# Kernel tuning notes

Measured on AMD Instinct MI355X. Metric: run time of the kernel, lower is better.

Reference implementation:

```python
import jax, jax.numpy as jnp
import numpy as np

B, NF, NT = 8, 4096, 4096
D_IN, D_HID, D_OUT, D_V = 3, 128, 32, 16


def mlp(x, W1, b1, W2, b2):
    # x: [B, N, D_IN] -> [B, N, D_OUT]
    h = jax.nn.relu(jnp.einsum('bni,ih->bnh', x, W1) + b1)
    return jnp.einsum('bnh,ho->bno', h, W2) + b2


def l1_cdist(a, b):
    # a: [B, N, d], b: [B, M, d] -> [B, N, M], sum_d |a-b|
    # scan over the small feature dim d to avoid a [B,N,M,d] intermediate
    aT = jnp.moveaxis(a, -1, 0)  # [d, B, N]
    bT = jnp.moveaxis(b, -1, 0)  # [d, B, M]

    def step(acc, ab):
        ai, bi = ab
        return acc + jnp.abs(ai[:, :, None] - bi[:, None, :]), None

    init = jnp.zeros((a.shape[0], a.shape[1], b.shape[1]), dtype=a.dtype)
    acc, _ = jax.lax.scan(step, init, (aT, bT))
    return acc


def setup_inputs() -> dict:
    key = jax.random.key(0)
    ks = jax.random.split(key, 11)
    s1 = 1.0 / np.sqrt(D_IN)
    s2 = 1.0 / np.sqrt(D_HID)
    return {
        'coords_f': jax.random.normal(ks[0], (B, NF, D_IN), jnp.float32),
        'values_f': jax.random.normal(ks[1], (B, NF, D_V), jnp.float32),
        'coords_t': jax.random.normal(ks[2], (B, NT, D_IN), jnp.float32),
        'Wk1': jax.random.uniform(ks[3], (D_IN, D_HID), jnp.float32, -s1, s1),
        'bk1': jax.random.uniform(ks[4], (D_HID,), jnp.float32, -s1, s1),
        'Wk2': jax.random.uniform(ks[5], (D_HID, D_OUT), jnp.float32, -s2, s2),
        'bk2': jax.random.uniform(ks[6], (D_OUT,), jnp.float32, -s2, s2),
        'Wq1': jax.random.uniform(ks[7], (D_IN, D_HID), jnp.float32, -s1, s1),
        'bq1': jax.random.uniform(ks[8], (D_HID,), jnp.float32, -s1, s1),
        'Wq2': jax.random.uniform(ks[9], (D_HID, D_OUT), jnp.float32, -s2, s2),
        'bq2': jax.random.uniform(ks[10], (D_OUT,), jnp.float32, -s2, s2),
    }


def reference(coords_f, values_f, coords_t, Wk1, bk1, Wk2, bk2, Wq1, bq1, Wq2, bq2):
    Wk = mlp(coords_f, Wk1, bk1, Wk2, bk2)  # [B, NF, D_OUT]
    Wq = mlp(coords_t, Wq1, bq1, Wq2, bq2)  # [B, NT, D_OUT]
    score = l1_cdist(Wk, Wq)                # [B, NF, NT]
    attn = jax.nn.softmax(-(score ** 2) / 2.0, axis=1)  # softmax over NF
    # 'bij,bik->bjk': [B,NF,NT] x [B,NF,V] -> [B,NT,V]
    return jnp.einsum('bij,bik->bjk', attn, values_f)
```

## Files before the change

### kernel.cpp

```cpp
#include <hip/hip_runtime.h>

#define B 8
#define NF 4096
#define NT 4096
#define D_HID 128
#define D_OUT 32
#define D_V 16
#define TILE_I 64

__device__ inline float fast_exp2(float x) {
#if __has_builtin(__builtin_amdgcn_exp2f)
  return __builtin_amdgcn_exp2f(x);
#else
  return exp2f(x);
#endif
}

__global__ __launch_bounds__(64) void mlp_kernel(
    const float* __restrict__ x, const float* __restrict__ W1,
    const float* __restrict__ b1, const float* __restrict__ W2,
    const float* __restrict__ b2, float* __restrict__ out) {
  __shared__ float sW1[3 * D_HID];
  __shared__ float sb1[D_HID];
  __shared__ float sW2[D_HID * D_OUT];
  __shared__ float sb2[D_OUT];
  const int tid = threadIdx.x;
  for (int idx = tid; idx < D_HID * D_OUT; idx += 64) sW2[idx] = W2[idx];
  for (int idx = tid; idx < 3 * D_HID; idx += 64) sW1[idx] = W1[idx];
  for (int idx = tid; idx < D_HID; idx += 64) sb1[idx] = b1[idx];
  if (tid < D_OUT) sb2[tid] = b2[tid];
  __syncthreads();

  const int t = blockIdx.x * 64 + tid;
  const float x0 = x[t * 3 + 0];
  const float x1 = x[t * 3 + 1];
  const float x2 = x[t * 3 + 2];
  float acc[D_OUT];
#pragma unroll
  for (int o = 0; o < D_OUT; ++o) acc[o] = sb2[o];
#pragma unroll 4
  for (int h = 0; h < D_HID; ++h) {
    float hv = fmaf(x2, sW1[2 * D_HID + h],
               fmaf(x1, sW1[1 * D_HID + h],
               fmaf(x0, sW1[0 * D_HID + h], sb1[h])));
    hv = fmaxf(hv, 0.0f);
    const float4* w2r = reinterpret_cast<const float4*>(&sW2[h * D_OUT]);
#pragma unroll
    for (int o4 = 0; o4 < D_OUT / 4; ++o4) {
      const float4 w = w2r[o4];
      acc[o4 * 4 + 0] = fmaf(hv, w.x, acc[o4 * 4 + 0]);
      acc[o4 * 4 + 1] = fmaf(hv, w.y, acc[o4 * 4 + 1]);
      acc[o4 * 4 + 2] = fmaf(hv, w.z, acc[o4 * 4 + 2]);
      acc[o4 * 4 + 3] = fmaf(hv, w.w, acc[o4 * 4 + 3]);
    }
  }
  float* op = out + (size_t)t * D_OUT;
#pragma unroll
  for (int o = 0; o < D_OUT; o += 4) {
    float4 w = make_float4(acc[o], acc[o + 1], acc[o + 2], acc[o + 3]);
    *reinterpret_cast<float4*>(op + o) = w;
  }
}

__global__ __launch_bounds__(256, 3) void attn_kernel(
    const float* __restrict__ Wk, const float* __restrict__ Wq,
    const float* __restrict__ Vf, float* __restrict__ partial,
    int nchunks, int chlen) {
  __shared__ float4 sTile[2][768];
  const int tid = threadIdx.x;
  const int j0 = blockIdx.x * 512 + tid;
  const int j1 = j0 + 256;
  const int b = blockIdx.y;
  const int c = blockIdx.z;
  const int i0 = c * chlen;
  const int ntiles = chlen / TILE_I;

  float q[2][D_OUT];
  {
    const float* qp0 = Wq + ((size_t)b * NT + j0) * D_OUT;
    const float* qp1 = Wq + ((size_t)b * NT + j1) * D_OUT;
#pragma unroll
    for (int d = 0; d < D_OUT; d += 4) {
      float4 t4 = *reinterpret_cast<const float4*>(qp0 + d);
      q[0][d + 0] = t4.x; q[0][d + 1] = t4.y; q[0][d + 2] = t4.z; q[0][d + 3] = t4.w;
      float4 u4 = *reinterpret_cast<const float4*>(qp1 + d);
      q[1][d + 0] = u4.x; q[1][d + 1] = u4.y; q[1][d + 2] = u4.z; q[1][d + 3] = u4.w;
    }
  }

  constexpr float C2 = -0.72134752044448170368f;

  float m0 = -1e30f, m1 = -1e30f;
  float l0 = 0.0f, l1 = 0.0f;
  float acc[2][D_V];
#pragma unroll
  for (int s = 0; s < 2; ++s)
#pragma unroll
    for (int k = 0; k < D_V; ++k) acc[s][k] = 0.0f;

  const float4* gK4 = reinterpret_cast<const float4*>(Wk + ((size_t)b * NF + i0) * D_OUT);
  const float4* gV4 = reinterpret_cast<const float4*>(Vf + ((size_t)b * NF + i0) * D_V);

  {
    float4 f0 = gK4[tid];
    float4 f1 = gK4[256 + tid];
    float4 f2 = gV4[tid];
    sTile[0][tid] = f0;
    sTile[0][256 + tid] = f1;
    sTile[0][512 + tid] = f2;
  }
  __syncthreads();

  for (int t = 0; t < ntiles; ++t) {
    const int cur = t & 1;
    float4 f0, f1, f2;
    const bool more = (t + 1 < ntiles);
    if (more) {
      f0 = gK4[(size_t)(t + 1) * 512 + tid];
      f1 = gK4[(size_t)(t + 1) * 512 + 256 + tid];
      f2 = gV4[(size_t)(t + 1) * 256 + tid];
    }
    const float4* kb4 = &sTile[cur][0];
    const float4* vb4 = &sTile[cur][512];
    for (int r = 0; r < TILE_I; ++r) {
      const float4 k0 = kb4[0];
      const float4 k1 = kb4[1];
      const float4 k2 = kb4[2];
      const float4 k3 = kb4[3];
      float a0 = fabsf(k0.x - q[0][0]);
      float b0 = fabsf(k0.x - q[1][0]);
      float a1 = fabsf(k0.y - q[0][1]);
      float b1 = fabsf(k0.y - q[1][1]);
      float a2 = fabsf(k0.z - q[0][2]);
      float b2 = fabsf(k0.z - q[1][2]);
      float a3 = fabsf(k0.w - q[0][3]);
      float b3 = fabsf(k0.w - q[1][3]);
      a0 += fabsf(k1.x - q[0][4]);  b0 += fabsf(k1.x - q[1][4]);
      a1 += fabsf(k1.y - q[0][5]);  b1 += fabsf(k1.y - q[1][5]);
      a2 += fabsf(k1.z - q[0][6]);  b2 += fabsf(k1.z - q[1][6]);
      a3 += fabsf(k1.w - q[0][7]);  b3 += fabsf(k1.w - q[1][7]);
      a0 += fabsf(k2.x - q[0][8]);  b0 += fabsf(k2.x - q[1][8]);
      a1 += fabsf(k2.y - q[0][9]);  b1 += fabsf(k2.y - q[1][9]);
      a2 += fabsf(k2.z - q[0][10]); b2 += fabsf(k2.z - q[1][10]);
      a3 += fabsf(k2.w - q[0][11]); b3 += fabsf(k2.w - q[1][11]);
      a0 += fabsf(k3.x - q[0][12]); b0 += fabsf(k3.x - q[1][12]);
      a1 += fabsf(k3.y - q[0][13]); b1 += fabsf(k3.y - q[1][13]);
      a2 += fabsf(k3.z - q[0][14]); b2 += fabsf(k3.z - q[1][14]);
      a3 += fabsf(k3.w - q[0][15]); b3 += fabsf(k3.w - q[1][15]);
      const float4 k4 = kb4[4];
      const float4 k5 = kb4[5];
      const float4 k6 = kb4[6];
      const float4 k7 = kb4[7];
      kb4 += 8;
      a0 += fabsf(k4.x - q[0][16]); b0 += fabsf(k4.x - q[1][16]);
      a1 += fabsf(k4.y - q[0][17]); b1 += fabsf(k4.y - q[1][17]);
      a2 += fabsf(k4.z - q[0][18]); b2 += fabsf(k4.z - q[1][18]);
      a3 += fabsf(k4.w - q[0][19]); b3 += fabsf(k4.w - q[1][19]);
      a0 += fabsf(k5.x - q[0][20]); b0 += fabsf(k5.x - q[1][20]);
      a1 += fabsf(k5.y - q[0][21]); b1 += fabsf(k5.y - q[1][21]);
      a2 += fabsf(k5.z - q[0][22]); b2 += fabsf(k5.z - q[1][22]);
      a3 += fabsf(k5.w - q[0][23]); b3 += fabsf(k5.w - q[1][23]);
      a0 += fabsf(k6.x - q[0][24]); b0 += fabsf(k6.x - q[1][24]);
      a1 += fabsf(k6.y - q[0][25]); b1 += fabsf(k6.y - q[1][25]);
      a2 += fabsf(k6.z - q[0][26]); b2 += fabsf(k6.z - q[1][26]);
      a3 += fabsf(k6.w - q[0][27]); b3 += fabsf(k6.w - q[1][27]);
      a0 += fabsf(k7.x - q[0][28]); b0 += fabsf(k7.x - q[1][28]);
      a1 += fabsf(k7.y - q[0][29]); b1 += fabsf(k7.y - q[1][29]);
      a2 += fabsf(k7.z - q[0][30]); b2 += fabsf(k7.z - q[1][30]);
      a3 += fabsf(k7.w - q[0][31]); b3 += fabsf(k7.w - q[1][31]);
      const float dist0 = (a0 + a1) + (a2 + a3);
      const float dist1 = (b0 + b1) + (b2 + b3);

      const float d20 = dist0 * dist0;
      const float d21 = dist1 * dist1;
      float parg0 = fmaf(C2, d20, -m0);
      float parg1 = fmaf(C2, d21, -m1);
      if (__any(fmaxf(parg0, parg1) > 4.0f)) {
        const float s20 = C2 * d20;
        const float mn0 = fmaxf(m0, s20);
        const float al0 = fast_exp2(m0 - mn0);
        l0 *= al0;
#pragma unroll
        for (int k = 0; k < D_V; ++k) acc[0][k] *= al0;
        m0 = mn0;
        parg0 = s20 - mn0;
        const float s21 = C2 * d21;
        const float mn1 = fmaxf(m1, s21);
        const float al1 = fast_exp2(m1 - mn1);
        l1 *= al1;
#pragma unroll
        for (int k = 0; k < D_V; ++k) acc[1][k] *= al1;
        m1 = mn1;
        parg1 = s21 - mn1;
      }
      const float p0 = fast_exp2(parg0);
      const float p1 = fast_exp2(parg1);
      l0 += p0;
      l1 += p1;

      {
        const float4 v0 = vb4[0];
        const float4 v1 = vb4[1];
        acc[0][0]  = fmaf(p0, v0.x, acc[0][0]);   acc[1][0]  = fmaf(p1, v0.x, acc[1][0]);
        acc[0][1]  = fmaf(p0, v0.y, acc[0][1]);   acc[1][1]  = fmaf(p1, v0.y, acc[1][1]);
        acc[0][2]  = fmaf(p0, v0.z, acc[0][2]);   acc[1][2]  = fmaf(p1, v0.z, acc[1][2]);
        acc[0][3]  = fmaf(p0, v0.w, acc[0][3]);   acc[1][3]  = fmaf(p1, v0.w, acc[1][3]);
        acc[0][4]  = fmaf(p0, v1.x, acc[0][4]);   acc[1][4]  = fmaf(p1, v1.x, acc[1][4]);
        acc[0][5]  = fmaf(p0, v1.y, acc[0][5]);   acc[1][5]  = fmaf(p1, v1.y, acc[1][5]);
        acc[0][6]  = fmaf(p0, v1.z, acc[0][6]);   acc[1][6]  = fmaf(p1, v1.z, acc[1][6]);
        acc[0][7]  = fmaf(p0, v1.w, acc[0][7]);   acc[1][7]  = fmaf(p1, v1.w, acc[1][7]);
      }
      {
        const float4 v2 = vb4[2];
        const float4 v3 = vb4[3];
        vb4 += 4;
        acc[0][8]  = fmaf(p0, v2.x, acc[0][8]);   acc[1][8]  = fmaf(p1, v2.x, acc[1][8]);
        acc[0][9]  = fmaf(p0, v2.y, acc[0][9]);   acc[1][9]  = fmaf(p1, v2.y, acc[1][9]);
        acc[0][10] = fmaf(p0, v2.z, acc[0][10]);  acc[1][10] = fmaf(p1, v2.z, acc[1][10]);
        acc[0][11] = fmaf(p0, v2.w, acc[0][11]);  acc[1][11] = fmaf(p1, v2.w, acc[1][11]);
        acc[0][12] = fmaf(p0, v3.x, acc[0][12]);  acc[1][12] = fmaf(p1, v3.x, acc[1][12]);
        acc[0][13] = fmaf(p0, v3.y, acc[0][13]);  acc[1][13] = fmaf(p1, v3.y, acc[1][13]);
        acc[0][14] = fmaf(p0, v3.z, acc[0][14]);  acc[1][14] = fmaf(p1, v3.z, acc[1][14]);
        acc[0][15] = fmaf(p0, v3.w, acc[0][15]);  acc[1][15] = fmaf(p1, v3.w, acc[1][15]);
      }
    }
    if (more) {
      const int nxt = cur ^ 1;
      sTile[nxt][tid] = f0;
      sTile[nxt][256 + tid] = f1;
      sTile[nxt][512 + tid] = f2;
    }
    __syncthreads();
  }

  const size_t fstride = (size_t)nchunks * B * NT;
  float* ps0 = partial + ((size_t)c * B + b) * NT + j0;
  float* ps1 = partial + ((size_t)c * B + b) * NT + j1;
  ps0[0] = m0;
  ps1[0] = m1;
  ps0[fstride] = l0;
  ps1[fstride] = l1;
#pragma unroll
  for (int k = 0; k < D_V; ++k) {
    ps0[(size_t)(2 + k) * fstride] = acc[0][k];
    ps1[(size_t)(2 + k) * fstride] = acc[1][k];
  }
}

__global__ __launch_bounds__(256) void combine_kernel(
    const float* __restrict__ partial, float* __restrict__ out, int nchunks) {
  const int t = blockIdx.x * 256 + threadIdx.x;
  const size_t fstride = (size_t)nchunks * B * NT;
  float M = -1e30f;
  for (int c = 0; c < nchunks; ++c)
    M = fmaxf(M, partial[(size_t)c * (B * NT) + t]);
  float L = 0.0f;
  float acc[D_V];
#pragma unroll
  for (int k = 0; k < D_V; ++k) acc[k] = 0.0f;
  for (int c = 0; c < nchunks; ++c) {
    const size_t base = (size_t)c * (B * NT) + t;
    const float w = fast_exp2(partial[base] - M);
    L = fmaf(w, partial[fstride + base], L);
#pragma unroll
    for (int k = 0; k < D_V; ++k)
      acc[k] = fmaf(w, partial[(size_t)(2 + k) * fstride + base], acc[k]);
  }
  const float inv = 1.0f / L;
  float* op = out + (size_t)t * D_V;
#pragma unroll
  for (int k = 0; k < D_V; ++k) op[k] = acc[k] * inv;
}

extern "C" void kernel_launch(void* const* d_in, const int* in_sizes, int n_in,
                              void* d_out, int out_size, void* d_ws, size_t ws_size,
                              hipStream_t stream) {
  const float* coords_f = (const float*)d_in[0];
  const float* values_f = (const float*)d_in[1];
  const float* coords_t = (const float*)d_in[2];
  const float* Wk1 = (const float*)d_in[3];
  const float* bk1 = (const float*)d_in[4];
  const float* Wk2 = (const float*)d_in[5];
  const float* bk2 = (const float*)d_in[6];
  const float* Wq1 = (const float*)d_in[7];
  const float* bq1 = (const float*)d_in[8];
  const float* Wq2 = (const float*)d_in[9];
  const float* bq2 = (const float*)d_in[10];
  float* out = (float*)d_out;

  float* Wk = (float*)d_ws;
  float* Wq = Wk + (size_t)B * NF * D_OUT;
  float* partial = Wq + (size_t)B * NT * D_OUT;

  const size_t fixed = (size_t)(B * NF * D_OUT + B * NT * D_OUT) * sizeof(float);
  int nchunks = 32;
  while (nchunks > 1 &&
         fixed + (size_t)B * NT * nchunks * 18 * sizeof(float) > ws_size)
    nchunks >>= 1;
  const int chlen = NF / nchunks;

  hipLaunchKernelGGL(mlp_kernel, dim3(B * NF / 64), dim3(64), 0, stream,
                     coords_f, Wk1, bk1, Wk2, bk2, Wk);
  hipLaunchKernelGGL(mlp_kernel, dim3(B * NT / 64), dim3(64), 0, stream,
                     coords_t, Wq1, bq1, Wq2, bq2, Wq);
  hipLaunchKernelGGL(attn_kernel, dim3(NT / 512, B, nchunks), dim3(256), 0, stream,
                     Wk, Wq, values_f, partial, nchunks, chlen);
  hipLaunchKernelGGL(combine_kernel, dim3(B * NT / 256), dim3(256), 0, stream,
                     partial, out, nchunks);
}
```

Measured before the change: 429.1 us.

## Split NF into 128-row chunks loaded once, dropping tile double-buffering

Each block now handles a fixed 128-row chunk of keys and values, loaded into shared memory once before the loop. This replaces the double-buffered 64-row tile pipeline and its per-tile barriers. The chunk count grows to 32 regardless of workspace size, which gives more blocks and parallelism but enlarges the partial buffer and the combine work. Occupancy hints are raised to 4 blocks per CU, and the combine kernel uses 128-thread blocks. The fixed chunk count also drops the workspace-size check, so a small workspace could overflow.

```diff
diff --git a/kernel.cpp b/kernel.cpp
--- a/kernel.cpp
+++ b/kernel.cpp
@@ -6,7 +6,7 @@
 #define D_HID 128
 #define D_OUT 32
 #define D_V 16
-#define TILE_I 64
+#define CHLEN 128
 
 __device__ inline float fast_exp2(float x) {
 #if __has_builtin(__builtin_amdgcn_exp2f)
@@ -62,29 +62,38 @@
   }
 }
 
-__global__ __launch_bounds__(256, 3) void attn_kernel(
+__global__ __launch_bounds__(256, 4) void attn_kernel(
     const float* __restrict__ Wk, const float* __restrict__ Wq,
     const float* __restrict__ Vf, float* __restrict__ partial,
-    int nchunks, int chlen) {
-  __shared__ float4 sTile[2][768];
+    int nchunks) {
+  __shared__ float4 sK[CHLEN * 8];
+  __shared__ float4 sV[CHLEN * 4];
   const int tid = threadIdx.x;
-  const int j0 = blockIdx.x * 512 + tid;
-  const int j1 = j0 + 256;
   const int b = blockIdx.y;
   const int c = blockIdx.z;
-  const int i0 = c * chlen;
-  const int ntiles = chlen / TILE_I;
+  const int i0 = c * CHLEN;
+  const int j0 = blockIdx.x * 512 + tid;
+
+  {
+    const float4* gK4 =
+        reinterpret_cast<const float4*>(Wk + ((size_t)b * NF + i0) * D_OUT);
+    const float4* gV4 =
+        reinterpret_cast<const float4*>(Vf + ((size_t)b * NF + i0) * D_V);
+#pragma unroll
+    for (int i = 0; i < 4; ++i) sK[tid + 256 * i] = gK4[tid + 256 * i];
+#pragma unroll
+    for (int i = 0; i < 2; ++i) sV[tid + 256 * i] = gV4[tid + 256 * i];
+  }
 
   float q[2][D_OUT];
-  {
-    const float* qp0 = Wq + ((size_t)b * NT + j0) * D_OUT;
-    const float* qp1 = Wq + ((size_t)b * NT + j1) * D_OUT;
+#pragma unroll
+  for (int s = 0; s < 2; ++s) {
+    const float* qp = Wq + ((size_t)b * NT + j0 + s * 256) * D_OUT;
 #pragma unroll
     for (int d = 0; d < D_OUT; d += 4) {
-      float4 t4 = *reinterpret_cast<const float4*>(qp0 + d);
-      q[0][d + 0] = t4.x; q[0][d + 1] = t4.y; q[0][d + 2] = t4.z; q[0][d + 3] = t4.w;
-      float4 u4 = *reinterpret_cast<const float4*>(qp1 + d);
-      q[1][d + 0] = u4.x; q[1][d + 1] = u4.y; q[1][d + 2] = u4.z; q[1][d + 3] = u4.w;
+      float4 t4 = *reinterpret_cast<const float4*>(qp + d);
+      q[s][d + 0] = t4.x; q[s][d + 1] = t4.y;
+      q[s][d + 2] = t4.z; q[s][d + 3] = t4.w;
     }
   }
 
@@ -98,158 +107,129 @@
 #pragma unroll
     for (int k = 0; k < D_V; ++k) acc[s][k] = 0.0f;
 
-  const float4* gK4 = reinterpret_cast<const float4*>(Wk + ((size_t)b * NF + i0) * D_OUT);
-  const float4* gV4 = reinterpret_cast<const float4*>(Vf + ((size_t)b * NF + i0) * D_V);
-
+  __syncthreads();
+
+  for (int r = 0; r < CHLEN; ++r) {
+    const float4* kp = &sK[r * 8];
+    const float4 k0 = kp[0];
+    const float4 k1 = kp[1];
+    const float4 k2 = kp[2];
+    const float4 k3 = kp[3];
+    float a0 = fabsf(k0.x - q[0][0]);
+    float b0 = fabsf(k0.x - q[1][0]);
+    float a1 = fabsf(k0.y - q[0][1]);
+    float b1 = fabsf(k0.y - q[1][1]);
+    float a2 = fabsf(k0.z - q[0][2]);
+    float b2 = fabsf(k0.z - q[1][2]);
+    float a3 = fabsf(k0.w - q[0][3]);
+    float b3 = fabsf(k0.w - q[1][3]);
+    a0 += fabsf(k1.x - q[0][4]);  b0 += fabsf(k1.x - q[1][4]);
+    a1 += fabsf(k1.y - q[0][5]);  b1 += fabsf(k1.y - q[1][5]);
+    a2 += fabsf(k1.z - q[0][6]);  b2 += fabsf(k1.z - q[1][6]);
+    a3 += fabsf(k1.w - q[0][7]);  b3 += fabsf(k1.w - q[1][7]);
+    a0 += fabsf(k2.x - q[0][8]);  b0 += fabsf(k2.x - q[1][8]);
+    a1 += fabsf(k2.y - q[0][9]);  b1 += fabsf(k2.y - q[1][9]);
+    a2 += fabsf(k2.z - q[0][10]); b2 += fabsf(k2.z - q[1][10]);
+    a3 += fabsf(k2.w - q[0][11]); b3 += fabsf(k2.w - q[1][11]);
+    a0 += fabsf(k3.x - q[0][12]); b0 += fabsf(k3.x - q[1][12]);
+    a1 += fabsf(k3.y - q[0][13]); b1 += fabsf(k3.y - q[1][13]);
+    a2 += fabsf(k3.z - q[0][14]); b2 += fabsf(k3.z - q[1][14]);
+    a3 += fabsf(k3.w - q[0][15]); b3 += fabsf(k3.w - q[1][15]);
+    const float4 k4 = kp[4];
+    const float4 k5 = kp[5];
+    const float4 k6 = kp[6];
+    const float4 k7 = kp[7];
+    a0 += fabsf(k4.x - q[0][16]); b0 += fabsf(k4.x - q[1][16]);
+    a1 += fabsf(k4.y - q[0][17]); b1 += fabsf(k4.y - q[1][17]);
+    a2 += fabsf(k4.z - q[0][18]); b2 += fabsf(k4.z - q[1][18]);
+    a3 += fabsf(k4.w - q[0][19]); b3 += fabsf(k4.w - q[1][19]);
+    a0 += fabsf(k5.x - q[0][20]); b0 += fabsf(k5.x - q[1][20]);
+    a1 += fabsf(k5.y - q[0][21]); b1 += fabsf(k5.y - q[1][21]);
+    a2 += fabsf(k5.z - q[0][22]); b2 += fabsf(k5.z - q[1][22]);
+    a3 += fabsf(k5.w - q[0][23]); b3 += fabsf(k5.w - q[1][23]);
+    a0 += fabsf(k6.x - q[0][24]); b0 += fabsf(k6.x - q[1][24]);
+    a1 += fabsf(k6.y - q[0][25]); b1 += fabsf(k6.y - q[1][25]);
+    a2 += fabsf(k6.z - q[0][26]); b2 += fabsf(k6.z - q[1][26]);
+    a3 += fabsf(k6.w - q[0][27]); b3 += fabsf(k6.w - q[1][27]);
+    a0 += fabsf(k7.x - q[0][28]); b0 += fabsf(k7.x - q[1][28]);
+    a1 += fabsf(k7.y - q[0][29]); b1 += fabsf(k7.y - q[1][29]);
+    a2 += fabsf(k7.z - q[0][30]); b2 += fabsf(k7.z - q[1][30]);
+    a3 += fabsf(k7.w - q[0][31]); b3 += fabsf(k7.w - q[1][31]);
+    const float dist0 = (a0 + a1) + (a2 + a3);
+    const float dist1 = (b0 + b1) + (b2 + b3);
+
+    const float d20 = dist0 * dist0;
+    const float d21 = dist1 * dist1;
+    float parg0 = fmaf(C2, d20, -m0);
+    float parg1 = fmaf(C2, d21, -m1);
+    if (__any(fmaxf(parg0, parg1) > 4.0f)) {
+      const float s20 = C2 * d20;
+      const float mn0 = fmaxf(m0, s20);
+      const float al0 = fast_exp2(m0 - mn0);
+      l0 *= al0;
+#pragma unroll
+      for (int k = 0; k < D_V; ++k) acc[0][k] *= al0;
+      m0 = mn0;
+      parg0 = s20 - mn0;
+      const float s21 = C2 * d21;
+      const float mn1 = fmaxf(m1, s21);
+      const float al1 = fast_exp2(m1 - mn1);
+      l1 *= al1;
+#pragma unroll
+      for (int k = 0; k < D_V; ++k) acc[1][k] *= al1;
+      m1 = mn1;
+      parg1 = s21 - mn1;
+    }
+    const float p0 = fast_exp2(parg0);
+    const float p1 = fast_exp2(parg1);
+    l0 += p0;
+    l1 += p1;
+
+    {
+      const float4 v0 = sV[r * 4 + 0];
+      const float4 v1 = sV[r * 4 + 1];
+      acc[0][0] = fmaf(p0, v0.x, acc[0][0]);  acc[1][0] = fmaf(p1, v0.x, acc[1][0]);
+      acc[0][1] = fmaf(p0, v0.y, acc[0][1]);  acc[1][1] = fmaf(p1, v0.y, acc[1][1]);
+      acc[0][2] = fmaf(p0, v0.z, acc[0][2]);  acc[1][2] = fmaf(p1, v0.z, acc[1][2]);
+      acc[0][3] = fmaf(p0, v0.w, acc[0][3]);  acc[1][3] = fmaf(p1, v0.w, acc[1][3]);
+      acc[0][4] = fmaf(p0, v1.x, acc[0][4]);  acc[1][4] = fmaf(p1, v1.x, acc[1][4]);
+      acc[0][5] = fmaf(p0, v1.y, acc[0][5]);  acc[1][5] = fmaf(p1, v1.y, acc[1][5]);
+      acc[0][6] = fmaf(p0, v1.z, acc[0][6]);  acc[1][6] = fmaf(p1, v1.z, acc[1][6]);
+      acc[0][7] = fmaf(p0, v1.w, acc[0][7]);  acc[1][7] = fmaf(p1, v1.w, acc[1][7]);
+    }
+    {
+      const float4 v2 = sV[r * 4 + 2];
+      const float4 v3 = sV[r * 4 + 3];
+      acc[0][8]  = fmaf(p0, v2.x, acc[0][8]);   acc[1][8]  = fmaf(p1, v2.x, acc[1][8]);
+      acc[0][9]  = fmaf(p0, v2.y, acc[0][9]);   acc[1][9]  = fmaf(p1, v2.y, acc[1][9]);
+      acc[0][10] = fmaf(p0, v2.z, acc[0][10]);  acc[1][10] = fmaf(p1, v2.z, acc[1][10]);
+      acc[0][11] = fmaf(p0, v2.w, acc[0][11]);  acc[1][11] = fmaf(p1, v2.w, acc[1][11]);
+      acc[0][12] = fmaf(p0, v3.x, acc[0][12]);  acc[1][12] = fmaf(p1, v3.x, acc[1][12]);
+      acc[0][13] = fmaf(p0, v3.y, acc[0][13]);  acc[1][13] = fmaf(p1, v3.y, acc[1][13]);
+      acc[0][14] = fmaf(p0, v3.z, acc[0][14]);  acc[1][14] = fmaf(p1, v3.z, acc[1][14]);
+      acc[0][15] = fmaf(p0, v3.w, acc[0][15]);  acc[1][15] = fmaf(p1, v3.w, acc[1][15]);
+    }
+  }
+
+  const size_t fstride = (size_t)nchunks * B * NT;
+  const size_t base = ((size_t)c * B + b) * NT;
   {
-    float4 f0 = gK4[tid];
-    float4 f1 = gK4[256 + tid];
-    float4 f2 = gV4[tid];
-    sTile[0][tid] = f0;
-    sTile[0][256 + tid] = f1;
-    sTile[0][512 + tid] = f2;
-  }
-  __syncthreads();
-
-  for (int t = 0; t < ntiles; ++t) {
-    const int cur = t & 1;
-    float4 f0, f1, f2;
-    const bool more = (t + 1 < ntiles);
-    if (more) {
-      f0 = gK4[(size_t)(t + 1) * 512 + tid];
-      f1 = gK4[(size_t)(t + 1) * 512 + 256 + tid];
-      f2 = gV4[(size_t)(t + 1) * 256 + tid];
-    }
-    const float4* kb4 = &sTile[cur][0];
-    const float4* vb4 = &sTile[cur][512];
-    for (int r = 0; r < TILE_I; ++r) {
-      const float4 k0 = kb4[0];
-      const float4 k1 = kb4[1];
-      const float4 k2 = kb4[2];
-      const float4 k3 = kb4[3];
-      float a0 = fabsf(k0.x - q[0][0]);
-      float b0 = fabsf(k0.x - q[1][0]);
-      float a1 = fabsf(k0.y - q[0][1]);
-      float b1 = fabsf(k0.y - q[1][1]);
-      float a2 = fabsf(k0.z - q[0][2]);
-      float b2 = fabsf(k0.z - q[1][2]);
-      float a3 = fabsf(k0.w - q[0][3]);
-      float b3 = fabsf(k0.w - q[1][3]);
-      a0 += fabsf(k1.x - q[0][4]);  b0 += fabsf(k1.x - q[1][4]);
-      a1 += fabsf(k1.y - q[0][5]);  b1 += fabsf(k1.y - q[1][5]);
-      a2 += fabsf(k1.z - q[0][6]);  b2 += fabsf(k1.z - q[1][6]);
-      a3 += fabsf(k1.w - q[0][7]);  b3 += fabsf(k1.w - q[1][7]);
-      a0 += fabsf(k2.x - q[0][8]);  b0 += fabsf(k2.x - q[1][8]);
-      a1 += fabsf(k2.y - q[0][9]);  b1 += fabsf(k2.y - q[1][9]);
-      a2 += fabsf(k2.z - q[0][10]); b2 += fabsf(k2.z - q[1][10]);
-      a3 += fabsf(k2.w - q[0][11]); b3 += fabsf(k2.w - q[1][11]);
-      a0 += fabsf(k3.x - q[0][12]); b0 += fabsf(k3.x - q[1][12]);
-      a1 += fabsf(k3.y - q[0][13]); b1 += fabsf(k3.y - q[1][13]);
-      a2 += fabsf(k3.z - q[0][14]); b2 += fabsf(k3.z - q[1][14]);
-      a3 += fabsf(k3.w - q[0][15]); b3 += fabsf(k3.w - q[1][15]);
-      const float4 k4 = kb4[4];
-      const float4 k5 = kb4[5];
-      const float4 k6 = kb4[6];
-      const float4 k7 = kb4[7];
-      kb4 += 8;
-      a0 += fabsf(k4.x - q[0][16]); b0 += fabsf(k4.x - q[1][16]);
-      a1 += fabsf(k4.y - q[0][17]); b1 += fabsf(k4.y - q[1][17]);
-      a2 += fabsf(k4.z - q[0][18]); b2 += fabsf(k4.z - q[1][18]);
-      a3 += fabsf(k4.w - q[0][19]); b3 += fabsf(k4.w - q[1][19]);
-      a0 += fabsf(k5.x - q[0][20]); b0 += fabsf(k5.x - q[1][20]);
-      a1 += fabsf(k5.y - q[0][21]); b1 += fabsf(k5.y - q[1][21]);
-      a2 += fabsf(k5.z - q[0][22]); b2 += fabsf(k5.z - q[1][22]);
-      a3 += fabsf(k5.w - q[0][23]); b3 += fabsf(k5.w - q[1][23]);
-      a0 += fabsf(k6.x - q[0][24]); b0 += fabsf(k6.x - q[1][24]);
-      a1 += fabsf(k6.y - q[0][25]); b1 += fabsf(k6.y - q[1][25]);
-      a2 += fabsf(k6.z - q[0][26]); b2 += fabsf(k6.z - q[1][26]);
-      a3 += fabsf(k6.w - q[0][27]); b3 += fabsf(k6.w - q[1][27]);
-      a0 += fabsf(k7.x - q[0][28]); b0 += fabsf(k7.x - q[1][28]);
-      a1 += fabsf(k7.y - q[0][29]); b1 += fabsf(k7.y - q[1][29]);
-      a2 += fabsf(k7.z - q[0][30]); b2 += fabsf(k7.z - q[1][30]);
-      a3 += fabsf(k7.w - q[0][31]); b3 += fabsf(k7.w - q[1][31]);
-      const float dist0 = (a0 + a1) + (a2 + a3);
-      const float dist1 = (b0 + b1) + (b2 + b3);
-
-      const float d20 = dist0 * dist0;
-      const float d21 = dist1 * dist1;
-      float parg0 = fmaf(C2, d20, -m0);
-      float parg1 = fmaf(C2, d21, -m1);
-      if (__any(fmaxf(parg0, parg1) > 4.0f)) {
-        const float s20 = C2 * d20;
-        const float mn0 = fmaxf(m0, s20);
-        const float al0 = fast_exp2(m0 - mn0);
-        l0 *= al0;
-#pragma unroll
-        for (int k = 0; k < D_V; ++k) acc[0][k] *= al0;
-        m0 = mn0;
-        parg0 = s20 - mn0;
-        const float s21 = C2 * d21;
-        const float mn1 = fmaxf(m1, s21);
-        const float al1 = fast_exp2(m1 - mn1);
-        l1 *= al1;
-#pragma unroll
-        for (int k = 0; k < D_V; ++k) acc[1][k] *= al1;
-        m1 = mn1;
-        parg1 = s21 - mn1;
-      }
-      const float p0 = fast_exp2(parg0);
-      const float p1 = fast_exp2(parg1);
-      l0 += p0;
-      l1 += p1;
-
-      {
-        const float4 v0 = vb4[0];
-        const float4 v1 = vb4[1];
-        acc[0][0]  = fmaf(p0, v0.x, acc[0][0]);   acc[1][0]  = fmaf(p1, v0.x, acc[1][0]);
-        acc[0][1]  = fmaf(p0, v0.y, acc[0][1]);   acc[1][1]  = fmaf(p1, v0.y, acc[1][1]);
-        acc[0][2]  = fmaf(p0, v0.z, acc[0][2]);   acc[1][2]  = fmaf(p1, v0.z, acc[1][2]);
-        acc[0][3]  = fmaf(p0, v0.w, acc[0][3]);   acc[1][3]  = fmaf(p1, v0.w, acc[1][3]);
-        acc[0][4]  = fmaf(p0, v1.x, acc[0][4]);   acc[1][4]  = fmaf(p1, v1.x, acc[1][4]);
-        acc[0][5]  = fmaf(p0, v1.y, acc[0][5]);   acc[1][5]  = fmaf(p1, v1.y, acc[1][5]);
-        acc[0][6]  = fmaf(p0, v1.z, acc[0][6]);   acc[1][6]  = fmaf(p1, v1.z, acc[1][6]);
-        acc[0][7]  = fmaf(p0, v1.w, acc[0][7]);   acc[1][7]  = fmaf(p1, v1.w, acc[1][7]);
-      }
-      {
-        const float4 v2 = vb4[2];
-        const float4 v3 = vb4[3];
-        vb4 += 4;
-        acc[0][8]  = fmaf(p0, v2.x, acc[0][8]);   acc[1][8]  = fmaf(p1, v2.x, acc[1][8]);
-        acc[0][9]  = fmaf(p0, v2.y, acc[0][9]);   acc[1][9]  = fmaf(p1, v2.y, acc[1][9]);
-        acc[0][10] = fmaf(p0, v2.z, acc[0][10]);  acc[1][10] = fmaf(p1, v2.z, acc[1][10]);
-        acc[0][11] = fmaf(p0, v2.w, acc[0][11]);  acc[1][11] = fmaf(p1, v2.w, acc[1][11]);
-        acc[0][12] = fmaf(p0, v3.x, acc[0][12]);  acc[1][12] = fmaf(p1, v3.x, acc[1][12]);
-        acc[0][13] = fmaf(p0, v3.y, acc[0][13]);  acc[1][13] = fmaf(p1, v3.y, acc[1][13]);
-        acc[0][14] = fmaf(p0, v3.z, acc[0][14]);  acc[1][14] = fmaf(p1, v3.z, acc[1][14]);
-        acc[0][15] = fmaf(p0, v3.w, acc[0][15]);  acc[1][15] = fmaf(p1, v3.w, acc[1][15]);
-      }
-    }
-    if (more) {
-      const int nxt = cur ^ 1;
-      sTile[nxt][tid] = f0;
-      sTile[nxt][256 + tid] = f1;
-      sTile[nxt][512 + tid] = f2;
-    }
-    __syncthreads();
-  }
-
-  const size_t fstride = (size_t)nchunks * B * NT;
-  float* ps0 = partial + ((size_t)c * B + b) * NT + j0;
-  float* ps1 = partial + ((size_t)c * B + b) * NT + j1;
-  ps0[0] = m0;
-  ps1[0] = m1;
-  ps0[fstride] = l0;
-  ps1[fstride] = l1;
-#pragma unroll
-  for (int k = 0; k < D_V; ++k) {
-    ps0[(size_t)(2 + k) * fstride] = acc[0][k];
-    ps1[(size_t)(2 + k) * fstride] = acc[1][k];
-  }
-}
-
-__global__ __launch_bounds__(256) void combine_kernel(
+    float* ps = partial + base + j0;
+    ps[0] = m0;
+    ps[fstride] = l0;
+#pragma unroll
+    for (int k = 0; k < D_V; ++k) ps[(size_t)(2 + k) * fstride] = acc[0][k];
+    float* pt = partial + base + j0 + 256;
+    pt[0] = m1;
+    pt[fstride] = l1;
+#pragma unroll
+    for (int k = 0; k < D_V; ++k) pt[(size_t)(2 + k) * fstride] = acc[1][k];
+  }
+}
+
+__global__ __launch_bounds__(128) void combine_kernel(
     const float* __restrict__ partial, float* __restrict__ out, int nchunks) {
-  const int t = blockIdx.x * 256 + threadIdx.x;
+  const int t = blockIdx.x * 128 + threadIdx.x;
   const size_t fstride = (size_t)nchunks * B * NT;
   float M = -1e30f;
   for (int c = 0; c < nchunks; ++c)
@@ -291,20 +271,14 @@
   float* Wk = (float*)d_ws;
   float* Wq = Wk + (size_t)B * NF * D_OUT;
   float* partial = Wq + (size_t)B * NT * D_OUT;
-
-  const size_t fixed = (size_t)(B * NF * D_OUT + B * NT * D_OUT) * sizeof(float);
-  int nchunks = 32;
-  while (nchunks > 1 &&
-         fixed + (size_t)B * NT * nchunks * 18 * sizeof(float) > ws_size)
-    nchunks >>= 1;
-  const int chlen = NF / nchunks;
+  const int nchunks = NF / CHLEN;
 
   hipLaunchKernelGGL(mlp_kernel, dim3(B * NF / 64), dim3(64), 0, stream,
                      coords_f, Wk1, bk1, Wk2, bk2, Wk);
   hipLaunchKernelGGL(mlp_kernel, dim3(B * NT / 64), dim3(64), 0, stream,
                      coords_t, Wq1, bq1, Wq2, bq2, Wq);
   hipLaunchKernelGGL(attn_kernel, dim3(NT / 512, B, nchunks), dim3(256), 0, stream,
-                     Wk, Wq, values_f, partial, nchunks, chlen);
-  hipLaunchKernelGGL(combine_kernel, dim3(B * NT / 256), dim3(256), 0, stream,
+                     Wk, Wq, values_f, partial, nchunks);
+  hipLaunchKernelGGL(combine_kernel, dim3(B * NT / 128), dim3(128), 0, stream,
                      partial, out, nchunks);
 }
```

Measured after the change: 691.7 us. 61.2% more time.
